# Kernel optimization log

Hardware: AMD Instinct MI355X
Metric: run time of the kernel (lower is better)

Reference implementation:

```python
import jax, jax.numpy as jnp
import numpy as np

B, C, E, H = 4, 2048, 1024, 16
D = E // H
EPS = 1e-5

def _layernorm(x, g, b):
    mu = jnp.mean(x, axis=-1, keepdims=True)
    var = jnp.mean(jnp.square(x - mu), axis=-1, keepdims=True)
    return (x - mu) * jax.lax.rsqrt(var + EPS) * g + b

def setup_inputs() -> dict:
    key = jax.random.key(0)
    ks = jax.random.split(key, 12)
    s = 1.0 / np.sqrt(E)
    return {
        "inputs": jax.random.normal(ks[0], (B, C, E), dtype=jnp.float32),
        "Wq": jax.random.normal(ks[1], (E, E), dtype=jnp.float32) * s,
        "bq": jnp.zeros((E,), dtype=jnp.float32),
        "Wk": jax.random.normal(ks[2], (E, E), dtype=jnp.float32) * s,
        "bk": jnp.zeros((E,), dtype=jnp.float32),
        "Wv": jax.random.normal(ks[3], (E, E), dtype=jnp.float32) * s,
        "bv": jnp.zeros((E,), dtype=jnp.float32),
        "g1": jnp.ones((E,), dtype=jnp.float32),
        "beta1": jnp.zeros((E,), dtype=jnp.float32),
        "g2": jnp.ones((E,), dtype=jnp.float32),
        "beta2": jnp.zeros((E,), dtype=jnp.float32),
        "W1": jax.random.normal(ks[4], (E, 4 * E), dtype=jnp.float32) * s,
        "bm1": jnp.zeros((4 * E,), dtype=jnp.float32),
        "W2": jax.random.normal(ks[5], (4 * E, E), dtype=jnp.float32) * (1.0 / np.sqrt(4 * E)),
        "bm2": jnp.zeros((E,), dtype=jnp.float32),
    }

def reference(inputs, Wq, bq, Wk, bk, Wv, bv, g1, beta1, g2, beta2, W1, bm1, W2, bm2):
    b, c, e = inputs.shape
    normed = _layernorm(inputs, g1, beta1)
    q = (normed @ Wq + bq).reshape(b, c, H, D).transpose(0, 2, 1, 3)  # [B,H,C,D]
    k = (normed @ Wk + bk).reshape(b, c, H, D).transpose(0, 2, 1, 3)
    v = (normed @ Wv + bv).reshape(b, c, H, D).transpose(0, 2, 1, 3)
    scores = jnp.einsum('bhqd,bhkd->bhqk', q, k) / np.sqrt(D).astype(np.float32)
    causal = jnp.triu(jnp.ones((c, c), dtype=bool), k=1)  # True above diagonal
    scores = jnp.where(causal, -jnp.inf, scores)
    probs = jax.nn.softmax(scores, axis=-1)
    attn = jnp.einsum('bhqk,bhkd->bhqd', probs, v)
    attn = attn.transpose(0, 2, 1, 3).reshape(b, c, e)
    out = inputs + attn
    h = _layernorm(out, g2, beta2)
    mlp = jax.nn.relu(h @ W1 + bm1) @ W2 + bm2
    return out + mlp
```

## Files before the change

### kernel.cpp

```cpp
#include <hip/hip_runtime.h>
#include <math.h>

#define B_ 4
#define C_ 2048
#define E_ 1024
#define H_ 16
#define D_ 64
#define ROWS_ (B_*C_)

typedef __bf16 bf16x8 __attribute__((ext_vector_type(8)));
typedef float f32x4 __attribute__((ext_vector_type(4)));

__device__ __forceinline__ float b2f(unsigned short u) {
  unsigned int x = ((unsigned int)u) << 16;
  return __builtin_bit_cast(float, x);
}
__device__ __forceinline__ unsigned short f2b(float f) {
  unsigned int x = __builtin_bit_cast(unsigned int, f);
  unsigned int r = (x + 0x7FFFu + ((x >> 16) & 1u)) >> 16;
  return (unsigned short)r;
}
__device__ __forceinline__ unsigned short tob(float f) { return f2b(f); }
__device__ __forceinline__ unsigned short tob(unsigned short u) { return u; }
__device__ __forceinline__ void store_out(float* p, float v) { *p = v; }
__device__ __forceinline__ void store_out(unsigned short* p, float v) { *p = f2b(v); }

__device__ __forceinline__ void async16(const void* g, void* l) {
  __builtin_amdgcn_global_load_lds(
      (__attribute__((address_space(1))) unsigned int*)g,
      (__attribute__((address_space(3))) unsigned int*)l, 16, 0, 0);
}

template <typename InT>
__global__ __launch_bounds__(256) void transpose64(
    const InT* __restrict__ in, unsigned short* __restrict__ out,
    int s_in, int s_out, int Hz, long zs_b, long zs_h, long zs_out)
{
  __shared__ unsigned short t[64][65];
  int z = blockIdx.z;
  long ib = (long)(z / Hz) * zs_b + (long)(z % Hz) * zs_h;
  long ob = (long)z * zs_out;
  int r0 = blockIdx.y * 64, c0 = blockIdx.x * 64;
  int lane = threadIdx.x & 63, grp = threadIdx.x >> 6;
  for (int i = grp; i < 64; i += 4)
    t[i][lane] = tob(in[ib + (long)(r0 + i) * s_in + c0 + lane]);
  __syncthreads();
  for (int i = grp; i < 64; i += 4)
    out[ob + (long)(c0 + i) * s_out + r0 + lane] = t[lane][i];
}

__global__ void concat_bias(const float* __restrict__ q,
                            const float* __restrict__ k,
                            const float* __restrict__ v,
                            float* __restrict__ o)
{
  int i = blockIdx.x * 256 + threadIdx.x;
  o[i] = (i < 1024) ? q[i] : (i < 2048) ? k[i - 1024] : v[i - 2048];
}

__global__ __launch_bounds__(256) void ln_kernel(
    const float* __restrict__ xin, const unsigned short* __restrict__ addend,
    const float* __restrict__ g, const float* __restrict__ beta,
    unsigned short* __restrict__ yout, float* __restrict__ out1)
{
  int row = blockIdx.x, tid = threadIdx.x;
  size_t base = (size_t)row * E_ + tid * 4;
  float4 xa = *(const float4*)(xin + base);
  float v0 = xa.x, v1 = xa.y, v2 = xa.z, v3 = xa.w;
  if (addend) {
    ushort4 aa = *(const ushort4*)(addend + base);
    v0 += b2f(aa.x); v1 += b2f(aa.y); v2 += b2f(aa.z); v3 += b2f(aa.w);
  }
  if (out1) {
    *(float4*)(out1 + base) = make_float4(v0, v1, v2, v3);
  }
  float s = v0 + v1 + v2 + v3;
  float sq = v0*v0 + v1*v1 + v2*v2 + v3*v3;
  #pragma unroll
  for (int off = 32; off >= 1; off >>= 1) {
    s  += __shfl_xor(s, off);
    sq += __shfl_xor(sq, off);
  }
  __shared__ float red[8];
  int wid = tid >> 6;
  if ((tid & 63) == 0) { red[wid] = s; red[4 + wid] = sq; }
  __syncthreads();
  s  = red[0] + red[1] + red[2] + red[3];
  sq = red[4] + red[5] + red[6] + red[7];
  float mu = s * (1.0f / E_);
  float var = sq * (1.0f / E_) - mu * mu;
  float rs = rsqrtf(var + 1e-5f);
  float4 ga = *(const float4*)(g + tid * 4);
  float4 ba = *(const float4*)(beta + tid * 4);
  ushort4 o;
  o.x = f2b((v0 - mu) * rs * ga.x + ba.x);
  o.y = f2b((v1 - mu) * rs * ga.y + ba.y);
  o.z = f2b((v2 - mu) * rs * ga.z + ba.z);
  o.w = f2b((v3 - mu) * rs * ga.w + ba.w);
  *(ushort4*)(yout + base) = o;
}

#define BARC() { asm volatile("" ::: "memory"); __builtin_amdgcn_s_barrier(); asm volatile("" ::: "memory"); }

#define MFMA_HALF(mh) do {                                                  \
  __builtin_amdgcn_s_setprio(1);                                            \
  _Pragma("unroll")                                                         \
  for (int mt_ = 0; mt_ < 4; ++mt_)                                         \
    _Pragma("unroll")                                                       \
    for (int nt_ = 0; nt_ < 4; ++nt_)                                       \
      acc[(mh)*4+mt_][nt_] = __builtin_amdgcn_mfma_f32_16x16x32_bf16(       \
          af[(mh)*4+mt_], bfr[nt_], acc[(mh)*4+mt_][nt_], 0, 0, 0);         \
  __builtin_amdgcn_s_setprio(0);                                            \
} while (0)

template <typename OutT>
__global__ __launch_bounds__(512, 2) void gemm256(
    const unsigned short* __restrict__ A, const unsigned short* __restrict__ Bt,
    const float* __restrict__ bias, const float* __restrict__ resid,
    OutT* __restrict__ Co, int M, int N, int K, int lda, int ldb,
    int relu, size_t zs)
{
  __shared__ __align__(16) unsigned short As[2][256 * 32];
  __shared__ __align__(16) unsigned short Bs[2][256 * 32];
  int tid = threadIdx.x, lane = tid & 63, wid = tid >> 6;
  int lane15 = lane & 15, quad = lane >> 4;
  int wm = wid >> 2, wn = wid & 3;

  int i = blockIdx.x;
  int xcd = i & 7, c = i >> 3;
  int bm = xcd * 4 + (c & 3);
  int bn = c >> 2;
  size_t koff = (size_t)blockIdx.z * K;
  int z0 = (blockIdx.z == 0);
  Co += (size_t)blockIdx.z * zs;

  int sr2 = tid >> 2, s2 = tid & 3;
  int gcolg = s2 ^ ((tid >> 2) & 3) ^ ((tid >> 4) & 3);
  const unsigned short* Ag = A + koff + (size_t)(bm * 256 + sr2) * lda + gcolg * 8;
  const unsigned short* Bg = Bt + koff + (size_t)(bn * 256 + sr2) * ldb + gcolg * 8;
  int dstb = wid * 512;

  int NT = K >> 5;

  f32x4 acc[8][4];
  #pragma unroll
  for (int m = 0; m < 8; ++m)
    #pragma unroll
    for (int n = 0; n < 4; ++n) acc[m][n] = 0.0f;

  auto stA = [&](int kt, int h) {
    async16(Ag + (size_t)(h * 128) * lda + kt * 32,
            &As[kt & 1][h * 4096 + dstb]);
  };
  auto stB = [&](int kt, int h) {
    async16(Bg + (size_t)(h * 128) * ldb + kt * 32,
            &Bs[kt & 1][h * 4096 + dstb]);
  };
  int rdoff = ((quad ^ ((lane15 & 3) ^ (lane15 >> 2))) * 8);

  stA(0, 0); stA(0, 1); stB(0, 0); stB(0, 1);
  stA(1, 0); stA(1, 1); stB(1, 0); stB(1, 1);
  asm volatile("s_waitcnt vmcnt(4)" ::: "memory");
  __builtin_amdgcn_s_barrier();

  for (int t = 0; t < NT; ++t) {
    const unsigned short* Ab = &As[t & 1][0];
    const unsigned short* Bb = &Bs[t & 1][0];
    bool more = (t + 2 < NT);
    bf16x8 af[8], bfr[4];
    #pragma unroll
    for (int m = 0; m < 8; ++m)
      af[m] = *(const bf16x8*)&Ab[(wm * 128 + m * 16 + lane15) * 32 + rdoff];
    #pragma unroll
    for (int n = 0; n < 4; ++n)
      bfr[n] = *(const bf16x8*)&Bb[(wn * 64 + n * 16 + lane15) * 32 + rdoff];
    BARC();
    asm volatile("s_waitcnt lgkmcnt(0)" ::: "memory");
    MFMA_HALF(0);
    BARC();
    if (more) { stA(t + 2, 0); stA(t + 2, 1); stB(t + 2, 0); stB(t + 2, 1); }
    MFMA_HALF(1);
    if (more) { asm volatile("s_waitcnt vmcnt(4)" ::: "memory"); }
    else      { asm volatile("s_waitcnt vmcnt(0)" ::: "memory"); }
    BARC();
  }

  #pragma unroll
  for (int nt = 0; nt < 4; ++nt) {
    int col = bn * 256 + wn * 64 + nt * 16 + lane15;
    float bv = (bias && z0) ? bias[col] : 0.0f;
    #pragma unroll
    for (int mt = 0; mt < 8; ++mt) {
      int row0 = bm * 256 + wm * 128 + mt * 16 + quad * 4;
      #pragma unroll
      for (int r = 0; r < 4; ++r) {
        float val = acc[mt][nt][r] + bv;
        if (relu) val = fmaxf(val, 0.0f);
        if (resid && z0) val += resid[(size_t)(row0 + r) * N + col];
        store_out(&Co[(size_t)(row0 + r) * N + col], val);
      }
    }
  }
}

__global__ __launch_bounds__(256) void add2(
    const float* __restrict__ p0, const float* __restrict__ p1,
    float* __restrict__ out)
{
  size_t i = ((size_t)blockIdx.x * 256 + threadIdx.x) * 4;
  float4 a = *(const float4*)(p0 + i);
  float4 b = *(const float4*)(p1 + i);
  *(float4*)(out + i) = make_float4(a.x + b.x, a.y + b.y, a.z + b.z, a.w + b.w);
}

__global__ __launch_bounds__(512) void attn_kernel(
    const unsigned short* __restrict__ qkv, const unsigned short* __restrict__ vt,
    unsigned short* __restrict__ attnb,
    float* __restrict__ opart0, float* __restrict__ opart1,
    float* __restrict__ lpart)
{
  __shared__ __align__(16) unsigned short Klds[64 * 64];
  __shared__ __align__(16) unsigned short Vlds[64 * 64];
  __shared__ __align__(16) unsigned short Plds[8][16 * 72];
  int tid = threadIdx.x, lane = tid & 63, widx = tid >> 6;
  int lane15 = lane & 15, quad = lane >> 4;

  int bx = blockIdx.x;
  int qblk, p, split;
  if (bx < 16) { qblk = 15 - (bx >> 1); p = bx & 1; split = 1; }
  else         { qblk = 23 - bx;        p = 0;      split = 0; }
  int ntiles = 2 * qblk + 2;
  int kt0 = (split && p) ? (qblk + 1) : 0;
  int kt1 = (split && !p) ? (qblk + 1) : ntiles;

  int bh = blockIdx.y;
  int b = bh >> 4, h = bh & 15;
  int q0w = qblk * 128 + widx * 16;

  const float QSCALE = 0.18033688011112042f;
  const unsigned short* qb = qkv + (size_t)(b * C_ + q0w + lane15) * 3072 + h * 64;
  bf16x8 qa0 = *(const bf16x8*)(qb + quad * 8);
  bf16x8 qa1 = *(const bf16x8*)(qb + 32 + quad * 8);
  #pragma unroll
  for (int j = 0; j < 8; ++j) {
    qa0[j] = (__bf16)((float)qa0[j] * QSCALE);
    qa1[j] = (__bf16)((float)qa1[j] * QSCALE);
  }

  float lsum[4];
  f32x4 o[4];
  #pragma unroll
  for (int r = 0; r < 4; ++r) lsum[r] = 0.0f;
  #pragma unroll
  for (int nt = 0; nt < 4; ++nt) o[nt] = 0.0f;

  int sr = tid >> 3, sc = tid & 7, sw = sr & 7;
  const unsigned short* kg = qkv + (size_t)(b * C_ + kt0 * 64 + sr) * 3072 + 1024 + h * 64 + (sc ^ sw) * 8;
  const unsigned short* vg = vt + (size_t)bh * 64 * 2048 + (size_t)sr * 2048 + (sc ^ sw) * 8 + kt0 * 64;
  unsigned short* kl = &Klds[sr * 64 + sc * 8];
  unsigned short* vl = &Vlds[sr * 64 + sc * 8];
  int swr = lane15 & 7;

  for (int kt = kt0; kt < kt1; ++kt) {
    int k0 = kt * 64;
    async16(kg, kl);
    async16(vg, vl);
    kg += (size_t)64 * 3072;
    vg += 64;
    __syncthreads();

    if (k0 <= q0w + 15) {
      f32x4 s[4];
      #pragma unroll
      for (int g = 0; g < 4; ++g) s[g] = 0.0f;
      #pragma unroll
      for (int g = 0; g < 4; ++g) {
        int row = g * 16 + lane15;
        bf16x8 kf0 = *(const bf16x8*)&Klds[row * 64 + ((quad ^ swr) * 8)];
        bf16x8 kf1 = *(const bf16x8*)&Klds[row * 64 + (((4 + quad) ^ swr) * 8)];
        s[g] = __builtin_amdgcn_mfma_f32_16x16x32_bf16(qa0, kf0, s[g], 0, 0, 0);
        s[g] = __builtin_amdgcn_mfma_f32_16x16x32_bf16(qa1, kf1, s[g], 0, 0, 0);
      }

      if (k0 + 63 > q0w) {
        #pragma unroll
        for (int g = 0; g < 4; ++g)
          #pragma unroll
          for (int r = 0; r < 4; ++r)
            if (k0 + g * 16 + lane15 > q0w + quad * 4 + r) s[g][r] = -3.0e38f;
      }

      float pv[4][4];
      #pragma unroll
      for (int g = 0; g < 4; ++g)
        #pragma unroll
        for (int r = 0; r < 4; ++r) pv[g][r] = exp2f(s[g][r]);
      #pragma unroll
      for (int r = 0; r < 4; ++r)
        lsum[r] += (pv[0][r] + pv[1][r]) + (pv[2][r] + pv[3][r]);

      __bf16* prow = (__bf16*)&Plds[widx][0];
      #pragma unroll
      for (int g = 0; g < 4; ++g)
        #pragma unroll
        for (int r = 0; r < 4; ++r)
          prow[(quad * 4 + r) * 72 + g * 16 + lane15] = (__bf16)pv[g][r];
      asm volatile("s_waitcnt lgkmcnt(0)" ::: "memory");
      bf16x8 pa0 = *(const bf16x8*)&Plds[widx][lane15 * 72 + quad * 8];
      bf16x8 pa1 = *(const bf16x8*)&Plds[widx][lane15 * 72 + 32 + quad * 8];

      #pragma unroll
      for (int nt = 0; nt < 4; ++nt) {
        int d = nt * 16 + lane15;
        bf16x8 vf0 = *(const bf16x8*)&Vlds[d * 64 + ((quad ^ swr) * 8)];
        bf16x8 vf1 = *(const bf16x8*)&Vlds[d * 64 + (((4 + quad) ^ swr) * 8)];
        o[nt] = __builtin_amdgcn_mfma_f32_16x16x32_bf16(pa0, vf0, o[nt], 0, 0, 0);
        o[nt] = __builtin_amdgcn_mfma_f32_16x16x32_bf16(pa1, vf1, o[nt], 0, 0, 0);
      }
    }
    __syncthreads();
  }

  #pragma unroll
  for (int off = 1; off <= 8; off <<= 1)
    #pragma unroll
    for (int r = 0; r < 4; ++r)
      lsum[r] += __shfl_xor(lsum[r], off);

  if (!split) {
    float rl[4];
    #pragma unroll
    for (int r = 0; r < 4; ++r) rl[r] = 1.0f / lsum[r];
    #pragma unroll
    for (int nt = 0; nt < 4; ++nt)
      #pragma unroll
      for (int r = 0; r < 4; ++r) {
        float val = o[nt][r] * rl[r];
        attnb[(size_t)(b * C_ + q0w + quad * 4 + r) * E_ + h * 64 + nt * 16 + lane15] = f2b(val);
      }
  } else {
    float* op = p ? opart1 : opart0;
    size_t rbase = (size_t)bh * 1024 + (q0w - 1024) + quad * 4;
    #pragma unroll
    for (int nt = 0; nt < 4; ++nt)
      #pragma unroll
      for (int r = 0; r < 4; ++r)
        op[(rbase + r) * 64 + nt * 16 + lane15] = o[nt][r];
    if (lane15 == 0) {
      float* lp = lpart + (size_t)p * 65536;
      #pragma unroll
      for (int r = 0; r < 4; ++r) lp[rbase + r] = lsum[r];
    }
  }
}

__global__ __launch_bounds__(256) void attn_combine(
    const float* __restrict__ opart0, const float* __restrict__ opart1,
    const float* __restrict__ lpart, unsigned short* __restrict__ attnb)
{
  size_t i = (size_t)blockIdx.x * 256 + threadIdx.x;
  int d = (int)(i & 63);
  size_t rowi = i >> 6;
  int bh = (int)(rowi >> 10), row = (int)(rowi & 1023);
  float ov = opart0[rowi * 64 + d] + opart1[rowi * 64 + d];
  float lv = lpart[rowi] + lpart[65536 + rowi];
  int b = bh >> 4, h = bh & 15;
  attnb[(size_t)(b * C_ + 1024 + row) * E_ + h * 64 + d] = f2b(ov / lv);
}

extern "C" void kernel_launch(void* const* d_in, const int* in_sizes, int n_in,
                              void* d_out, int out_size, void* d_ws, size_t ws_size,
                              hipStream_t stream)
{
  const float* x   = (const float*)d_in[0];
  const float* Wq  = (const float*)d_in[1];
  const float* bq  = (const float*)d_in[2];
  const float* Wk  = (const float*)d_in[3];
  const float* bk  = (const float*)d_in[4];
  const float* Wv  = (const float*)d_in[5];
  const float* bv  = (const float*)d_in[6];
  const float* g1  = (const float*)d_in[7];
  const float* be1 = (const float*)d_in[8];
  const float* g2  = (const float*)d_in[9];
  const float* be2 = (const float*)d_in[10];
  const float* W1  = (const float*)d_in[11];
  const float* bm1 = (const float*)d_in[12];
  const float* W2  = (const float*)d_in[13];
  const float* bm2 = (const float*)d_in[14];

  char* ws = (char*)d_ws;
  float*          part0 = (float*)(ws + 0);
  unsigned short* norm1 = (unsigned short*)(ws + 0);
  unsigned short* wT    = (unsigned short*)(ws + 16777216);
  unsigned short* w1T   = (unsigned short*)(ws + 23068672);
  float*          biasq = (float*)(ws + 39845888);
  unsigned short* qkv   = (unsigned short*)(ws + 39858176);
  unsigned short* vtb   = (unsigned short*)(ws + 90189824);
  unsigned short* mid   = (unsigned short*)(ws + 39858176);
  unsigned short* attnb = (unsigned short*)(ws + 106967040);
  float*          out1  = (float*)(ws + 123744256);
  unsigned short* w2T   = (unsigned short*)(ws + 157298688);
  float*          part1 = (float*)(ws + 165687296);
  float*          opart0 = (float*)(ws + 165687296);
  float*          opart1 = (float*)(ws + 123744256);
  float*          lpartb = (float*)(ws + 0);
  size_t part_zs = ((size_t)165687296) / 4;

  transpose64<float><<<dim3(16, 16, 1), 256, 0, stream>>>(Wq, wT,               1024, 1024, 1, 0, 0, 0);
  transpose64<float><<<dim3(16, 16, 1), 256, 0, stream>>>(Wk, wT + 1024 * 1024, 1024, 1024, 1, 0, 0, 0);
  transpose64<float><<<dim3(16, 16, 1), 256, 0, stream>>>(Wv, wT + 2048 * 1024, 1024, 1024, 1, 0, 0, 0);
  transpose64<float><<<dim3(64, 16, 1), 256, 0, stream>>>(W1, w1T, 4096, 1024, 1, 0, 0, 0);
  transpose64<float><<<dim3(16, 64, 1), 256, 0, stream>>>(W2, w2T, 1024, 4096, 1, 0, 0, 0);
  concat_bias<<<12, 256, 0, stream>>>(bq, bk, bv, biasq);

  ln_kernel<<<ROWS_, 256, 0, stream>>>(x, nullptr, g1, be1, norm1, nullptr);

  gemm256<unsigned short><<<dim3(384, 1, 1), 512, 0, stream>>>(
      norm1, wT, biasq, nullptr, qkv, 8192, 3072, 1024, 1024, 1024, 0, 0);

  transpose64<unsigned short><<<dim3(1, 32, 64), 256, 0, stream>>>(
      qkv + 2048, vtb, 3072, 2048, 16, (long)C_ * 3072, 64, (long)64 * 2048);

  attn_kernel<<<dim3(24, 64), 512, 0, stream>>>(qkv, vtb, attnb, opart0, opart1, lpartb);
  attn_combine<<<16384, 256, 0, stream>>>(opart0, opart1, lpartb, attnb);

  ln_kernel<<<ROWS_, 256, 0, stream>>>(x, attnb, g2, be2, norm1, out1);

  gemm256<unsigned short><<<dim3(512, 1, 1), 512, 0, stream>>>(
      norm1, w1T, bm1, nullptr, mid, 8192, 4096, 1024, 1024, 1024, 1, 0);

  gemm256<float><<<dim3(128, 1, 2), 512, 0, stream>>>(
      mid, w2T, bm2, out1, part0, 8192, 1024, 2048, 4096, 4096, 0, part_zs);
  add2<<<8192, 256, 0, stream>>>(part0, part1, (float*)d_out);
}
```

Measured before the change: 602.9 us.

## Double GEMM K-tile to 64 with single-barrier prefetch and quarter-fragment MFMA

The bf16 GEMM kernel now stages 64-wide K tiles instead of 32-wide ones, using an 8-way XOR swizzle to match, and drops from two barriers per iteration to one. The next tile is prefetched at the top of each iteration with a one-tile lookahead (previously two). A-fragments are loaded in quarters interleaved with MFMA groups, which cuts register pressure. The aim is to halve loop and barrier overhead per unit of K. The cost is double the LDS per block (128 KB), which likely allows only one block per CU despite launch_bounds(512,2), and leaves less latency hiding for global loads.

```diff
diff --git a/kernel.cpp b/kernel.cpp
--- a/kernel.cpp
+++ b/kernel.cpp
@@ -102,14 +102,14 @@
 
 #define BARC() { asm volatile("" ::: "memory"); __builtin_amdgcn_s_barrier(); asm volatile("" ::: "memory"); }
 
-#define MFMA_HALF(mh) do {                                                  \
+#define MFMA_Q(mh) do {                                                     \
   __builtin_amdgcn_s_setprio(1);                                            \
   _Pragma("unroll")                                                         \
   for (int mt_ = 0; mt_ < 4; ++mt_)                                         \
     _Pragma("unroll")                                                       \
     for (int nt_ = 0; nt_ < 4; ++nt_)                                       \
       acc[(mh)*4+mt_][nt_] = __builtin_amdgcn_mfma_f32_16x16x32_bf16(       \
-          af[(mh)*4+mt_], bfr[nt_], acc[(mh)*4+mt_][nt_], 0, 0, 0);         \
+          af[mt_], bfr[nt_], acc[(mh)*4+mt_][nt_], 0, 0, 0);                \
   __builtin_amdgcn_s_setprio(0);                                            \
 } while (0)
 
@@ -120,8 +120,8 @@
     OutT* __restrict__ Co, int M, int N, int K, int lda, int ldb,
     int relu, size_t zs)
 {
-  __shared__ __align__(16) unsigned short As[2][256 * 32];
-  __shared__ __align__(16) unsigned short Bs[2][256 * 32];
+  __shared__ __align__(16) unsigned short As[2][256 * 64];
+  __shared__ __align__(16) unsigned short Bs[2][256 * 64];
   int tid = threadIdx.x, lane = tid & 63, wid = tid >> 6;
   int lane15 = lane & 15, quad = lane >> 4;
   int wm = wid >> 2, wn = wid & 3;
@@ -134,13 +134,13 @@
   int z0 = (blockIdx.z == 0);
   Co += (size_t)blockIdx.z * zs;
 
-  int sr2 = tid >> 2, s2 = tid & 3;
-  int gcolg = s2 ^ ((tid >> 2) & 3) ^ ((tid >> 4) & 3);
-  const unsigned short* Ag = A + koff + (size_t)(bm * 256 + sr2) * lda + gcolg * 8;
-  const unsigned short* Bg = Bt + koff + (size_t)(bn * 256 + sr2) * ldb + gcolg * 8;
+  int sr = tid >> 3, sc = tid & 7;
+  int gcol = (sc ^ (sr & 7)) * 8;
+  const unsigned short* Ag = A + koff + (size_t)(bm * 256 + sr) * lda + gcol;
+  const unsigned short* Bg = Bt + koff + (size_t)(bn * 256 + sr) * ldb + gcol;
   int dstb = wid * 512;
 
-  int NT = K >> 5;
+  int NT = K >> 6;
 
   f32x4 acc[8][4];
   #pragma unroll
@@ -148,40 +148,55 @@
     #pragma unroll
     for (int n = 0; n < 4; ++n) acc[m][n] = 0.0f;
 
-  auto stA = [&](int kt, int h) {
-    async16(Ag + (size_t)(h * 128) * lda + kt * 32,
-            &As[kt & 1][h * 4096 + dstb]);
+  auto stage = [&](int kt) {
+    unsigned short* Ad = &As[kt & 1][dstb];
+    unsigned short* Bd = &Bs[kt & 1][dstb];
+    const unsigned short* Asrc = Ag + kt * 64;
+    const unsigned short* Bsrc = Bg + kt * 64;
+    #pragma unroll
+    for (int h = 0; h < 4; ++h) {
+      async16(Asrc + (size_t)(h * 64) * lda, Ad + h * 4096);
+      async16(Bsrc + (size_t)(h * 64) * ldb, Bd + h * 4096);
+    }
   };
-  auto stB = [&](int kt, int h) {
-    async16(Bg + (size_t)(h * 128) * ldb + kt * 32,
-            &Bs[kt & 1][h * 4096 + dstb]);
-  };
-  int rdoff = ((quad ^ ((lane15 & 3) ^ (lane15 >> 2))) * 8);
-
-  stA(0, 0); stA(0, 1); stB(0, 0); stB(0, 1);
-  stA(1, 0); stA(1, 1); stB(1, 0); stB(1, 1);
-  asm volatile("s_waitcnt vmcnt(4)" ::: "memory");
+  int rsw = lane15 & 7;
+
+  stage(0);
+  asm volatile("s_waitcnt vmcnt(0)" ::: "memory");
   __builtin_amdgcn_s_barrier();
 
   for (int t = 0; t < NT; ++t) {
     const unsigned short* Ab = &As[t & 1][0];
     const unsigned short* Bb = &Bs[t & 1][0];
-    bool more = (t + 2 < NT);
-    bf16x8 af[8], bfr[4];
-    #pragma unroll
-    for (int m = 0; m < 8; ++m)
-      af[m] = *(const bf16x8*)&Ab[(wm * 128 + m * 16 + lane15) * 32 + rdoff];
+    if (t + 1 < NT) stage(t + 1);
+    __builtin_amdgcn_sched_barrier(0);
+    bf16x8 af[4], bfr[4];
+    #pragma unroll
+    for (int m = 0; m < 4; ++m)
+      af[m] = *(const bf16x8*)&Ab[(wm * 128 + m * 16 + lane15) * 64 + ((quad ^ rsw) * 8)];
     #pragma unroll
     for (int n = 0; n < 4; ++n)
-      bfr[n] = *(const bf16x8*)&Bb[(wn * 64 + n * 16 + lane15) * 32 + rdoff];
-    BARC();
-    asm volatile("s_waitcnt lgkmcnt(0)" ::: "memory");
-    MFMA_HALF(0);
-    BARC();
-    if (more) { stA(t + 2, 0); stA(t + 2, 1); stB(t + 2, 0); stB(t + 2, 1); }
-    MFMA_HALF(1);
-    if (more) { asm volatile("s_waitcnt vmcnt(4)" ::: "memory"); }
-    else      { asm volatile("s_waitcnt vmcnt(0)" ::: "memory"); }
+      bfr[n] = *(const bf16x8*)&Bb[(wn * 64 + n * 16 + lane15) * 64 + ((quad ^ rsw) * 8)];
+    MFMA_Q(0);
+    __builtin_amdgcn_sched_barrier(0);
+    #pragma unroll
+    for (int m = 0; m < 4; ++m)
+      af[m] = *(const bf16x8*)&Ab[(wm * 128 + 64 + m * 16 + lane15) * 64 + ((quad ^ rsw) * 8)];
+    MFMA_Q(1);
+    __builtin_amdgcn_sched_barrier(0);
+    #pragma unroll
+    for (int m = 0; m < 4; ++m)
+      af[m] = *(const bf16x8*)&Ab[(wm * 128 + m * 16 + lane15) * 64 + (((4 + quad) ^ rsw) * 8)];
+    #pragma unroll
+    for (int n = 0; n < 4; ++n)
+      bfr[n] = *(const bf16x8*)&Bb[(wn * 64 + n * 16 + lane15) * 64 + (((4 + quad) ^ rsw) * 8)];
+    MFMA_Q(0);
+    __builtin_amdgcn_sched_barrier(0);
+    #pragma unroll
+    for (int m = 0; m < 4; ++m)
+      af[m] = *(const bf16x8*)&Ab[(wm * 128 + 64 + m * 16 + lane15) * 64 + (((4 + quad) ^ rsw) * 8)];
+    MFMA_Q(1);
+    asm volatile("s_waitcnt vmcnt(0)" ::: "memory");
     BARC();
   }
 
```

Result: faster. 565.9 us (-6.1%).
